# Kernel optimization log

Hardware: AMD Instinct MI355X
Metric: run time of the kernel (lower is better)

## Reference

```python
import jax, jax.numpy as jnp
import numpy as np

EPS = 1e-5  # torch BatchNorm2d default eps (eval mode with running stats)


def bn(x, g, b, m, v):
    # x: [B,C,H,W]; per-channel affine batchnorm in inference form
    return (x - m[:, None, None]) * (g[:, None, None] / jnp.sqrt(v[:, None, None] + EPS)) + b[:, None, None]


def self_attn(x, Wq, bq, Wk, bk, Wv, bv, rel_h, rel_w):
    # x: [B,C,H,W]; Wq/Wk/Wv: [C,C] (1x1 convs); rel_h: [C,H]; rel_w: [C,W]
    B, C, H, W = x.shape
    N = H * W
    q = jnp.einsum('oc,bchw->bohw', Wq, x).reshape(B, C, N) + bq[None, :, None]
    k = jnp.einsum('oc,bchw->bohw', Wk, x).reshape(B, C, N) + bk[None, :, None]
    v = jnp.einsum('oc,bchw->bohw', Wv, x).reshape(B, C, N) + bv[None, :, None]
    energy = jnp.einsum('bcn,bcm->bnm', q, k)                      # content: Q^T K
    pos = (rel_h[:, :, None] + rel_w[:, None, :]).reshape(C, N)    # [C, H*W]
    energy = energy + jnp.einsum('bcn,cm->bnm', q, pos)            # rel-pos bias term
    attn = jax.nn.softmax(energy, axis=-1)                         # [B,N,N]
    out = jnp.einsum('bcm,bnm->bcn', v, attn)                      # V @ attn^T
    return out.reshape(B, C, H, W)


def conv3x3(x, w):
    return jax.lax.conv_general_dilated(x, w, (1, 1), 'SAME',
                                        dimension_numbers=('NCHW', 'OIHW', 'NCHW'))


def setup_inputs() -> dict:
    key = jax.random.key(0)
    B, C, H, W, NH = 32, 512, 16, 16, 5
    ks = jax.random.split(key, 32)
    f = lambda i, shape, s=1.0: jax.random.normal(ks[i], shape, jnp.float32) * s
    inp = {
        'x0': f(0, (B, C, H, W)), 'x1': f(1, (B, C, H, W)), 'x2': f(2, (B, C, H, W)),
        'x3': f(3, (B, C, H, W)), 'x': f(4, (B, C, H, W)),
        'qW': f(5, (NH, C, C), 0.02), 'qB': f(6, (NH, C), 0.02),
        'kW': f(7, (NH, C, C), 0.02), 'kB': f(8, (NH, C), 0.02),
        'vW': f(9, (NH, C, C), 0.02), 'vB': f(10, (NH, C), 0.02),
        'relH': f(11, (NH, C, H)), 'relW': f(12, (NH, C, W)),
        'msw_W': f(13, (NH - 1, NH * C), 0.02),
        'msw_g': jnp.ones((NH - 1,)), 'msw_b': jnp.zeros((NH - 1,)),
        'msw_m': jnp.zeros((NH - 1,)), 'msw_v': jnp.ones((NH - 1,)),
        'fus_W': f(14, (C, C, 3, 3), 0.02),
        'fus_g': jnp.ones((C,)), 'fus_b': jnp.zeros((C,)),
        'fus_m': jnp.zeros((C,)), 'fus_v': jnp.ones((C,)),
        'top_g': jnp.ones((C,)), 'top_b': jnp.zeros((C,)),
        'top_m': jnp.zeros((C,)), 'top_v': jnp.ones((C,)),
        'h': 16, 'w': 16,
    }
    return inp


def reference(x0, x1, x2, x3, x, qW, qB, kW, kB, vW, vB, relH, relW,
              msw_W, msw_g, msw_b, msw_m, msw_v,
              fus_W, fus_g, fus_b, fus_m, fus_v,
              top_g, top_b, top_m, top_v, h, w):
    B, C, H, W = x.shape
    xs = jnp.stack([x0, x1, x2, x3, x])                            # [5,B,C,H,W]
    outs = jax.vmap(self_attn)(xs, qW, qB, kW, kB, vW, vB, relH, relW)  # [5,B,C,H,W]
    cat = outs.transpose(1, 0, 2, 3, 4).reshape(B, 5 * C, H, W)
    weights = jax.nn.sigmoid(bn(jnp.einsum('oc,bchw->bohw', msw_W, cat),
                                msw_g, msw_b, msw_m, msw_v))        # [B,4,H,W]
    x_ms = (weights[:, 0:1] * outs[0] + weights[:, 1:2] * outs[1]
            + weights[:, 2:3] * outs[2] + weights[:, 3:4] * outs[3] + outs[4])
    x_ms = jax.nn.relu(bn(conv3x3(x_ms, fus_W), fus_g, fus_b, fus_m, fus_v))
    out = jax.nn.relu(bn(x_ms + x, top_g, top_b, top_m, top_v))
    return out
```

## Files before the change

### kernel.cpp

```cpp
#include <hip/hip_runtime.h>
#include <cstdint>

using bf16x8  = __attribute__((ext_vector_type(8))) __bf16;
using f32x4   = __attribute__((ext_vector_type(4))) float;
using ushort8 = __attribute__((ext_vector_type(8))) unsigned short;

#define EPSN 1e-5f

__device__ __forceinline__ void gld16(const void* g, void* l) {
  __builtin_amdgcn_global_load_lds((const __attribute__((address_space(1))) void*)g,
                                   (__attribute__((address_space(3))) void*)l, 16, 0, 0);
}

__device__ __forceinline__ ushort f2bf(float f) {
  __bf16 h = (__bf16)f;
  return __builtin_bit_cast(unsigned short, h);
}
__device__ __forceinline__ float bf2f(ushort u) {
  union { uint32_t u; float f; } v; v.u = ((uint32_t)u) << 16; return v.f;
}

__device__ __forceinline__ void gemm_core(const ushort* __restrict__ Ag,
                                          const ushort* __restrict__ Bg,
                                          int ldk, int ksteps,
                                          ushort* As, ushort* Bs,
                                          f32x4 (&acc)[4][4]) {
  const int t = threadIdx.x, lane = t & 63, w = t >> 6;
  const int wr = w >> 1, wc = w & 1;
  for (int kt = 0; kt < ksteps; ++kt) {
    const int kbase = kt * 64;
#pragma unroll
    for (int p = 0; p < 4; ++p) {
      int q = p * 256 + t;
      int row = q >> 3, slot = q & 7;
      int srcs = slot ^ (row & 7);
      gld16(Ag + (size_t)row * ldk + kbase + srcs * 8, As + (p * 256 + w * 64) * 8);
      gld16(Bg + (size_t)row * ldk + kbase + srcs * 8, Bs + (p * 256 + w * 64) * 8);
    }
    __syncthreads();
#pragma unroll
    for (int kk = 0; kk < 2; ++kk) {
      bf16x8 af[4], bfv[4];
#pragma unroll
      for (int i = 0; i < 4; ++i) {
        int ra = wr * 64 + i * 16 + (lane & 15);
        int sa = (kk * 4 + (lane >> 4)) ^ (ra & 7);
        af[i] = *(const bf16x8*)(As + ra * 64 + sa * 8);
        int rb = wc * 64 + i * 16 + (lane & 15);
        int sb = (kk * 4 + (lane >> 4)) ^ (rb & 7);
        bfv[i] = *(const bf16x8*)(Bs + rb * 64 + sb * 8);
      }
#pragma unroll
      for (int i = 0; i < 4; ++i)
#pragma unroll
        for (int j = 0; j < 4; ++j)
          acc[i][j] = __builtin_amdgcn_mfma_f32_16x16x32_bf16(af[i], bfv[j], acc[i][j], 0, 0, 0);
    }
    __syncthreads();
  }
}

__global__ __launch_bounds__(256) void k_pre(const float* __restrict__ x0,
                                             const float* __restrict__ x1,
                                             const float* __restrict__ x2,
                                             const float* __restrict__ x3,
                                             const float* __restrict__ x4,
                                             const float* __restrict__ qW,
                                             const float* __restrict__ kW,
                                             const float* __restrict__ vW,
                                             const float* __restrict__ relH,
                                             const float* __restrict__ relW,
                                             ushort* __restrict__ xT,
                                             ushort* __restrict__ Wb,
                                             ushort* __restrict__ posb) {
  __shared__ float tile[64][65];
  int bid = blockIdx.x;
  const int t = threadIdx.x;
  if (bid < 5120) {
    const int nt4 = bid & 3;  bid >>= 2;
    const int ct  = bid & 7;  bid >>= 3;
    const int b   = bid & 31; bid >>= 5;
    const int ix  = bid;
    const float* xs = ix == 0 ? x0 : ix == 1 ? x1 : ix == 2 ? x2 : ix == 3 ? x3 : x4;
    const float* src = xs + ((size_t)b * 512 + ct * 64) * 256 + nt4 * 64;
    const int col = t & 63, rq = t >> 6;
#pragma unroll
    for (int rr = 0; rr < 16; ++rr) {
      int row = rr * 4 + rq;
      tile[row][col] = src[(size_t)row * 256 + col];
    }
    __syncthreads();
    ushort* dst = xT + ((size_t)(ix * 32 + b) * 256 + nt4 * 64) * 512 + ct * 64;
#pragma unroll
    for (int rr = 0; rr < 16; ++rr) {
      int nrow = rr * 4 + rq;
      dst[(size_t)nrow * 512 + col] = f2bf(tile[col][nrow]);
    }
  } else if (bid < 8960) {
    int idx = (bid - 5120) * 256 + t;
    int gi = idx * 4;
    int sel = gi / 1310720;
    int off = gi - sel * 1310720;
    const float* src = sel == 0 ? qW : (sel == 1 ? kW : vW);
    float4 vv = *(const float4*)(src + off);
    int h = off / 262144, rest = off - h * 262144;
    ushort4 o;
    o.x = f2bf(vv.x); o.y = f2bf(vv.y); o.z = f2bf(vv.z); o.w = f2bf(vv.w);
    *(ushort4*)(Wb + (size_t)(h * 3 + sel) * 262144 + rest) = o;
  } else {
    int idx8 = (bid - 8960) * 256 + t;
    int e0 = idx8 * 8;
    int c0 = e0 & 511, m = (e0 >> 9) & 255, h = e0 >> 17;
    ushort8 o;
#pragma unroll
    for (int e = 0; e < 8; ++e) {
      int c = c0 + e;
      o[e] = f2bf(relH[((size_t)h * 512 + c) * 16 + (m >> 4)] +
                  relW[((size_t)h * 512 + c) * 16 + (m & 15)]);
    }
    *(ushort8*)(posb + e0) = o;
  }
}

__global__ __launch_bounds__(512, 2) void k_qkv2(const ushort* __restrict__ Wb,
                                                 const ushort* __restrict__ xT,
                                                 const ushort* __restrict__ posb,
                                                 const float* __restrict__ qB,
                                                 const float* __restrict__ kB,
                                                 const float* __restrict__ vB,
                                                 ushort* __restrict__ qT,
                                                 ushort* __restrict__ kpT,
                                                 ushort* __restrict__ vv) {
  extern __shared__ ushort ls[];
  const int t = threadIdx.x, lane = t & 63;
  const int w = t >> 6, wm = w >> 2, wn = w & 3, g = lane >> 4, l = lane & 15;
  int bid = blockIdx.x;
  bid = (bid & 7) * 120 + (bid >> 3);
  const int h = bid / 192;
  const int r = bid % 192;

  const ushort* Ag;
  const ushort* Bg;
  const bool partA = r < 128;
  int pt = 0, nt = 0, mt = 0, ntv = 0;
  if (partA) {
    pt = r >> 2; nt = r & 3;
    Ag = xT + ((size_t)h * 8192 + pt * 256) * 512;
    const int sel = nt < 2 ? 0 : 1;
    Bg = Wb + ((size_t)(h * 3 + sel) * 512 + (nt & 1) * 256) * 512;
  } else {
    const int r2 = r - 128;
    mt = r2 >> 5; ntv = r2 & 31;
    Ag = Wb + ((size_t)(h * 3 + 2) * 512 + mt * 256) * 512;
    Bg = xT + ((size_t)h * 8192 + ntv * 256) * 512;
  }

  f32x4 acc[8][4];
#pragma unroll
  for (int i = 0; i < 8; ++i)
#pragma unroll
    for (int j = 0; j < 4; ++j) acc[i][j] = f32x4{0.f, 0.f, 0.f, 0.f};

#define QKV_STAGE(tt, slot)                                                    \
  {                                                                            \
    const int kb_ = (tt) * 32;                                                 \
    ushort* sa_ = ls + (slot) * 8192;                                          \
    ushort* sb_ = ls + 32768 + (slot) * 8192;                                  \
    _Pragma("unroll")                                                          \
    for (int p_ = 0; p_ < 2; ++p_) {                                           \
      int q_ = p_ * 512 + t;                                                   \
      int row_ = q_ >> 2, s4_ = q_ & 3;                                        \
      int src_ = s4_ ^ ((row_ ^ (row_ >> 2)) & 3);                             \
      gld16(Ag + (size_t)row_ * 512 + kb_ + src_ * 8, sa_ + q_ * 8);           \
      gld16(Bg + (size_t)row_ * 512 + kb_ + src_ * 8, sb_ + q_ * 8);           \
    }                                                                          \
  }

#define QKV_COMPUTE(slot)                                                      \
  {                                                                            \
    ushort* sa_ = ls + (slot) * 8192;                                          \
    ushort* sb_ = ls + 32768 + (slot) * 8192;                                  \
    bf16x8 bfv[4], af[8];                                                      \
    _Pragma("unroll")                                                          \
    for (int j_ = 0; j_ < 4; ++j_) {                                           \
      int rb_ = wn * 64 + j_ * 16 + l;                                         \
      int sb2_ = g ^ ((rb_ ^ (rb_ >> 2)) & 3);                                 \
      bfv[j_] = *(const bf16x8*)(sb_ + rb_ * 32 + sb2_ * 8);                   \
    }                                                                          \
    _Pragma("unroll")                                                          \
    for (int i_ = 0; i_ < 8; ++i_) {                                           \
      int ra_ = wm * 128 + i_ * 16 + l;                                        \
      int sa2_ = g ^ ((ra_ ^ (ra_ >> 2)) & 3);                                 \
      af[i_] = *(const bf16x8*)(sa_ + ra_ * 32 + sa2_ * 8);                    \
    }                                                                          \
    asm volatile("s_waitcnt lgkmcnt(0)" ::: "memory");                         \
    __builtin_amdgcn_sched_barrier(0);                                         \
    __builtin_amdgcn_s_setprio(1);                                             \
    _Pragma("unroll")                                                          \
    for (int i_ = 0; i_ < 8; ++i_)                                             \
      _Pragma("unroll")                                                        \
      for (int j_ = 0; j_ < 4; ++j_)                                           \
        acc[i_][j_] = __builtin_amdgcn_mfma_f32_16x16x32_bf16(af[i_], bfv[j_], \
                                                              acc[i_][j_], 0, 0, 0); \
    __builtin_amdgcn_s_setprio(0);                                             \
  }

  QKV_STAGE(0, 0);
  QKV_STAGE(1, 1);
  for (int tt = 0; tt < 14; ++tt) {
    QKV_STAGE(tt + 2, (tt + 2) & 3);
    __builtin_amdgcn_sched_barrier(0);
    asm volatile("s_waitcnt vmcnt(8)" ::: "memory");
    __builtin_amdgcn_s_barrier();
    __builtin_amdgcn_sched_barrier(0);
    QKV_COMPUTE(tt & 3);
  }
  __builtin_amdgcn_sched_barrier(0);
  asm volatile("s_waitcnt vmcnt(4)" ::: "memory");
  __builtin_amdgcn_s_barrier();
  __builtin_amdgcn_sched_barrier(0);
  QKV_COMPUTE(2);
  __builtin_amdgcn_sched_barrier(0);
  asm volatile("s_waitcnt vmcnt(0)" ::: "memory");
  __builtin_amdgcn_s_barrier();
  __builtin_amdgcn_sched_barrier(0);
  QKV_COMPUTE(3);
  __builtin_amdgcn_sched_barrier(0);
  __syncthreads();

  ushort(*Cs)[272] = (ushort(*)[272])ls;
  if (partA) {
    const bool isq = nt < 2;
    const float* bias = (isq ? qB : kB) + (size_t)h * 512 + (nt & 1) * 256;
    ushort* dst = isq ? qT : kpT;
    float bj[4];
#pragma unroll
    for (int j = 0; j < 4; ++j) bj[j] = bias[wn * 64 + j * 16 + l];
#pragma unroll
    for (int R = 0; R < 2; ++R) {
      if (wm == R) {
#pragma unroll
        for (int i = 0; i < 8; ++i)
#pragma unroll
          for (int j = 0; j < 4; ++j)
#pragma unroll
            for (int rr = 0; rr < 4; ++rr)
              Cs[i * 16 + g * 4 + rr][wn * 64 + j * 16 + l] = f2bf(acc[i][j][rr] + bj[j]);
      }
      __syncthreads();
#pragma unroll
      for (int it = 0; it < 8; ++it) {
        int lin = it * 512 + t;
        int row = lin >> 5, cc8 = (lin & 31) * 8;
        ushort8 cv = *(const ushort8*)&Cs[row][cc8];
        if (!isq) {
          ushort8 pv = *(const ushort8*)(posb + ((size_t)h * 256 + R * 128 + row) * 512 +
                                         (nt & 1) * 256 + cc8);
#pragma unroll
          for (int e = 0; e < 8; ++e) cv[e] = f2bf(bf2f(cv[e]) + bf2f(pv[e]));
        }
        *(ushort8*)(dst + ((size_t)h * 8192 + pt * 256 + R * 128 + row) * 512 +
                    (nt & 1) * 256 + cc8) = cv;
      }
      if (R == 0) __syncthreads();
    }
  } else {
    const float* bias = vB + (size_t)h * 512 + mt * 256;
#pragma unroll
    for (int R = 0; R < 2; ++R) {
      if (wm == R) {
#pragma unroll
        for (int i = 0; i < 8; ++i) {
          float4 b4 = *(const float4*)(bias + R * 128 + i * 16 + g * 4);
#pragma unroll
          for (int j = 0; j < 4; ++j)
#pragma unroll
            for (int rr = 0; rr < 4; ++rr)
              Cs[i * 16 + g * 4 + rr][wn * 64 + j * 16 + l] =
                  f2bf(acc[i][j][rr] + ((const float*)&b4)[rr]);
        }
      }
      __syncthreads();
#pragma unroll
      for (int it = 0; it < 8; ++it) {
        int lin = it * 512 + t;
        int row = lin >> 5, cc8 = (lin & 31) * 8;
        ushort8 cv = *(const ushort8*)&Cs[row][cc8];
        *(ushort8*)(vv + (((size_t)(h * 32 + ntv)) * 512 + mt * 256 + R * 128 + row) * 256 +
                    cc8) = cv;
      }
      if (R == 0) __syncthreads();
    }
  }
#undef QKV_STAGE
#undef QKV_COMPUTE
}

__global__ __launch_bounds__(256) void k_attn(const ushort* __restrict__ qT,
                                              const ushort* __restrict__ kpT,
                                              const float* __restrict__ fusW,
                                              ushort* __restrict__ attn,
                                              ushort* __restrict__ Wconv) {
  __shared__ ushort sm[20480];
  __shared__ float red[4][64];
  __shared__ float comb[64];
  int bid = blockIdx.x;
  const int t = threadIdx.x;
  if (bid >= 640) {
    int p = (bid - 640) * 256 + t;
    const float* src = fusW + (size_t)p * 9;
    float vv[9];
#pragma unroll
    for (int s = 0; s < 9; ++s) vv[s] = src[s];
#pragma unroll
    for (int s = 0; s < 9; ++s) Wconv[(size_t)s * 262144 + p] = f2bf(vv[s]);
    return;
  }
  bid = (bid & 7) * 80 + (bid >> 3);
  const int rt = bid & 3;
  const int hb = bid >> 2;
  ushort* As = sm;
  ushort* Bs = sm + 4096;
  const ushort* Ag = qT + ((size_t)hb * 256 + rt * 64) * 512;
  const ushort* Bg = kpT + (size_t)hb * 256 * 512;
  const int lane = t & 63, w = t >> 6, g = lane >> 4, l = lane & 15;

  f32x4 acc[4][4];
#pragma unroll
  for (int i = 0; i < 4; ++i)
#pragma unroll
    for (int j = 0; j < 4; ++j) acc[i][j] = f32x4{0.f, 0.f, 0.f, 0.f};

  for (int kt = 0; kt < 8; ++kt) {
    const int kbase = kt * 64;
#pragma unroll
    for (int p = 0; p < 2; ++p) {
      int q = p * 256 + t;
      int row = q >> 3, slot = q & 7, srcs = slot ^ (row & 7);
      gld16(Ag + (size_t)row * 512 + kbase + srcs * 8, As + (p * 256 + w * 64) * 8);
    }
#pragma unroll
    for (int p = 0; p < 8; ++p) {
      int q = p * 256 + t;
      int row = q >> 3, slot = q & 7, srcs = slot ^ (row & 7);
      gld16(Bg + (size_t)row * 512 + kbase + srcs * 8, Bs + (p * 256 + w * 64) * 8);
    }
    __syncthreads();
#pragma unroll
    for (int kk = 0; kk < 2; ++kk) {
      bf16x8 af[4], bfv[4];
#pragma unroll
      for (int i = 0; i < 4; ++i) {
        int ra = i * 16 + l;
        int sa = (kk * 4 + g) ^ (ra & 7);
        af[i] = *(const bf16x8*)(As + ra * 64 + sa * 8);
        int rb = w * 64 + i * 16 + l;
        int sb = (kk * 4 + g) ^ (rb & 7);
        bfv[i] = *(const bf16x8*)(Bs + rb * 64 + sb * 8);
      }
#pragma unroll
      for (int i = 0; i < 4; ++i)
#pragma unroll
        for (int j = 0; j < 4; ++j)
          acc[i][j] = __builtin_amdgcn_mfma_f32_16x16x32_bf16(af[i], bfv[j], acc[i][j], 0, 0, 0);
    }
    __syncthreads();
  }

#pragma unroll
  for (int i = 0; i < 4; ++i)
#pragma unroll
    for (int rr = 0; rr < 4; ++rr) {
      float v = fmaxf(fmaxf(acc[i][0][rr], acc[i][1][rr]), fmaxf(acc[i][2][rr], acc[i][3][rr]));
#pragma unroll
      for (int m = 1; m < 16; m <<= 1) v = fmaxf(v, __shfl_xor(v, m));
      if (l == 0) red[w][i * 16 + g * 4 + rr] = v;
    }
  __syncthreads();
  if (t < 64) comb[t] = fmaxf(fmaxf(red[0][t], red[1][t]), fmaxf(red[2][t], red[3][t]));
  __syncthreads();
#pragma unroll
  for (int i = 0; i < 4; ++i)
#pragma unroll
    for (int rr = 0; rr < 4; ++rr) {
      float mx = comb[i * 16 + g * 4 + rr];
      float s = 0.f;
#pragma unroll
      for (int j = 0; j < 4; ++j) {
        float e = expf(acc[i][j][rr] - mx);
        acc[i][j][rr] = e;
        s += e;
      }
#pragma unroll
      for (int m = 1; m < 16; m <<= 1) s += __shfl_xor(s, m);
      if (l == 0) red[w][i * 16 + g * 4 + rr] = s;
    }
  __syncthreads();
  if (t < 64) comb[t] = red[0][t] + red[1][t] + red[2][t] + red[3][t];
  __syncthreads();
  ushort(*P)[260] = (ushort(*)[260])sm;
#pragma unroll
  for (int i = 0; i < 4; ++i)
#pragma unroll
    for (int rr = 0; rr < 4; ++rr) {
      int row = i * 16 + g * 4 + rr;
      float inv = 1.f / comb[row];
#pragma unroll
      for (int j = 0; j < 4; ++j)
        P[row][w * 64 + j * 16 + l] = f2bf(acc[i][j][rr] * inv);
    }
  __syncthreads();
  ushort* Arow = attn + (size_t)hb * 65536 + (size_t)rt * 16384;
#pragma unroll
  for (int it = 0; it < 8; ++it) {
    int lin = it * 256 + t;
    int row = lin >> 5, c8 = (lin & 31) * 8;
    ushort8 cv = *(const ushort8*)&P[row][c8];
    *(ushort8*)(Arow + (size_t)row * 256 + c8) = cv;
  }
}

__global__ __launch_bounds__(256) void k_pv(const ushort* __restrict__ attn,
                                            const ushort* __restrict__ vv,
                                            ushort* __restrict__ OT) {
  __shared__ ushort lds[128 * 148];
  ushort* As = lds;
  ushort* Bs = lds + 8192;
  int bid = blockIdx.x;
  bid = (bid & 7) * 160 + (bid >> 3);
  const int nt = bid & 3; bid >>= 2;
  const int mt = bid & 1; bid >>= 1;
  const size_t hb = (size_t)bid;
  const ushort* Ag = attn + (hb * 256 + mt * 128) * 256;
  const ushort* Bg = vv + (hb * 512 + nt * 128) * 256;
  f32x4 acc[4][4];
#pragma unroll
  for (int i = 0; i < 4; ++i)
#pragma unroll
    for (int j = 0; j < 4; ++j) acc[i][j] = f32x4{0.f, 0.f, 0.f, 0.f};
  gemm_core(Ag, Bg, 256, 4, As, Bs, acc);
  const int t = threadIdx.x, lane = t & 63, w = t >> 6;
  const int wr = w >> 1, wc = w & 1, g = lane >> 4, l = lane & 15;
  ushort(*Cs)[148] = (ushort(*)[148])lds;
#pragma unroll
  for (int i = 0; i < 4; ++i)
#pragma unroll
    for (int j = 0; j < 4; ++j)
#pragma unroll
      for (int rr = 0; rr < 4; ++rr)
        Cs[wr * 64 + i * 16 + g * 4 + rr][wc * 64 + j * 16 + l] = f2bf(acc[i][j][rr]);
  __syncthreads();
#pragma unroll
  for (int it = 0; it < 8; ++it) {
    int lin = it * 256 + t;
    int row = lin >> 4, cc = (lin & 15) * 8;
    ushort8 cv = *(const ushort8*)&Cs[row][cc];
    *(ushort8*)(OT + (hb * 256 + mt * 128 + row) * 512 + nt * 128 + cc) = cv;
  }
}

__global__ __launch_bounds__(256) void k_weights(const ushort* __restrict__ OT,
                                                 const float* __restrict__ mswW,
                                                 const float* __restrict__ mg,
                                                 const float* __restrict__ mb,
                                                 const float* __restrict__ mm,
                                                 const float* __restrict__ mv,
                                                 ushort* __restrict__ xmsT) {
  __shared__ float msw[10240];
  const int t = threadIdx.x, lane = t & 63, w = t >> 6;
#pragma unroll
  for (int it = 0; it < 10; ++it) {
    int idx = it * 1024 + t * 4;
    *(float4*)(msw + idx) = *(const float4*)(mswW + idx);
  }
  __syncthreads();
  const size_t pix = (size_t)blockIdx.x * 4 + w;
  float o[5][2][4];
#pragma unroll
  for (int h = 0; h < 5; ++h)
#pragma unroll
    for (int hf = 0; hf < 2; ++hf) {
      ushort4 v = *(const ushort4*)(OT + ((size_t)h * 8192 + pix) * 512 + hf * 256 + lane * 4);
      o[h][hf][0] = bf2f(v.x); o[h][hf][1] = bf2f(v.y);
      o[h][hf][2] = bf2f(v.z); o[h][hf][3] = bf2f(v.w);
    }
  float a[4] = {0.f, 0.f, 0.f, 0.f};
#pragma unroll
  for (int j = 0; j < 4; ++j)
#pragma unroll
    for (int h = 0; h < 5; ++h)
#pragma unroll
      for (int hf = 0; hf < 2; ++hf) {
        float4 m4 = *(const float4*)(msw + j * 2560 + h * 512 + hf * 256 + lane * 4);
        a[j] += m4.x * o[h][hf][0] + m4.y * o[h][hf][1] +
                m4.z * o[h][hf][2] + m4.w * o[h][hf][3];
      }
#pragma unroll
  for (int m = 1; m < 64; m <<= 1) {
    a[0] += __shfl_xor(a[0], m); a[1] += __shfl_xor(a[1], m);
    a[2] += __shfl_xor(a[2], m); a[3] += __shfl_xor(a[3], m);
  }
  float wj[4];
#pragma unroll
  for (int j = 0; j < 4; ++j) {
    float val = (a[j] - mm[j]) * (mg[j] * rsqrtf(mv[j] + EPSN)) + mb[j];
    wj[j] = 1.f / (1.f + expf(-val));
  }
#pragma unroll
  for (int hf = 0; hf < 2; ++hf) {
    float r0 = wj[0] * o[0][hf][0] + wj[1] * o[1][hf][0] + wj[2] * o[2][hf][0] + wj[3] * o[3][hf][0] + o[4][hf][0];
    float r1 = wj[0] * o[0][hf][1] + wj[1] * o[1][hf][1] + wj[2] * o[2][hf][1] + wj[3] * o[3][hf][1] + o[4][hf][1];
    float r2 = wj[0] * o[0][hf][2] + wj[1] * o[1][hf][2] + wj[2] * o[2][hf][2] + wj[3] * o[3][hf][2] + o[4][hf][2];
    float r3 = wj[0] * o[0][hf][3] + wj[1] * o[1][hf][3] + wj[2] * o[2][hf][3] + wj[3] * o[3][hf][3] + o[4][hf][3];
    ushort4 pk; pk.x = f2bf(r0); pk.y = f2bf(r1); pk.z = f2bf(r2); pk.w = f2bf(r3);
    *(ushort4*)(xmsT + pix * 512 + hf * 256 + lane * 4) = pk;
  }
}

__global__ __launch_bounds__(256) void k_conv(const ushort* __restrict__ Wconv,
                                              const ushort* __restrict__ xmsT,
                                              float* __restrict__ y1a,
                                              float* __restrict__ y1b) {
  __shared__ ushort As3[3 * 128 * 64];
  __shared__ ushort xp[180 * 76];
  int bid = blockIdx.x;
  bid = (bid & 7) * 64 + (bid >> 3);
  const int ntl = bid & 1; bid >>= 1;
  const int mt = bid & 3;  bid >>= 2;
  const int halfk = bid & 1; bid >>= 1;
  const int bb = bid;
  const int y0 = ntl * 8;
  const int t = threadIdx.x, lane = t & 63, w = t >> 6, wr = w >> 1, wc = w & 1;
  f32x4 acc[4][4];
#pragma unroll
  for (int i = 0; i < 4; ++i)
#pragma unroll
    for (int j = 0; j < 4; ++j) acc[i][j] = f32x4{0.f, 0.f, 0.f, 0.f};

  for (int cb = halfk * 4; cb < halfk * 4 + 4; ++cb) {
    __syncthreads();
    for (int u = t; u < 1440; u += 256) {
      int slot = u & 7;
      int xpi = (u >> 3) % 18;
      int rl = u / 144;
      int yg = y0 - 1 + rl, xg = xpi - 1;
      uint4 val = make_uint4(0, 0, 0, 0);
      if (yg >= 0 && yg < 16 && (unsigned)xg < 16u)
        val = *(const uint4*)(xmsT + ((size_t)bb * 256 + yg * 16 + xg) * 512 + cb * 64 + slot * 8);
      *(uint4*)(xp + (rl * 18 + xpi) * 76 + slot * 8) = val;
    }
    for (int dy = 0; dy < 3; ++dy) {
#pragma unroll
      for (int dx = 0; dx < 3; ++dx)
#pragma unroll
        for (int p = 0; p < 4; ++p) {
          int q = p * 256 + t;
          int row = q >> 3, slot = q & 7, srcs = slot ^ (row & 7);
          gld16(Wconv + ((size_t)(dy * 3 + dx) * 512 + mt * 128 + row) * 512 + cb * 64 + srcs * 8,
                As3 + dx * 8192 + (p * 256 + w * 64) * 8);
        }
      __syncthreads();
#pragma unroll
      for (int dx = 0; dx < 3; ++dx)
#pragma unroll
        for (int kk = 0; kk < 2; ++kk) {
          bf16x8 af[4], bfv[4];
#pragma unroll
          for (int i = 0; i < 4; ++i) {
            int ra = wr * 64 + i * 16 + (lane & 15);
            int sa = (kk * 4 + (lane >> 4)) ^ (ra & 7);
            af[i] = *(const bf16x8*)(As3 + dx * 8192 + ra * 64 + sa * 8);
            int nl = wc * 64 + i * 16 + (lane & 15);
            int pp = ((nl >> 4) + dy) * 18 + (nl & 15) + dx;
            bfv[i] = *(const bf16x8*)(xp + pp * 76 + (kk * 4 + (lane >> 4)) * 8);
          }
#pragma unroll
          for (int i = 0; i < 4; ++i)
#pragma unroll
            for (int j = 0; j < 4; ++j)
              acc[i][j] = __builtin_amdgcn_mfma_f32_16x16x32_bf16(af[i], bfv[j], acc[i][j], 0, 0, 0);
        }
      __syncthreads();
    }
  }
  float* yp = halfk ? y1b : y1a;
  const int o0 = mt * 128 + wr * 64 + ((lane >> 4) << 2);
  const int n0 = ntl * 128 + wc * 64 + (lane & 15);
#pragma unroll
  for (int i = 0; i < 4; ++i)
#pragma unroll
    for (int j = 0; j < 4; ++j)
#pragma unroll
      for (int rr = 0; rr < 4; ++rr) {
        int o = o0 + i * 16 + rr, n = n0 + j * 16;
        yp[((size_t)bb * 512 + o) * 256 + n] = acc[i][j][rr];
      }
}

__global__ __launch_bounds__(256) void k_top(const float* __restrict__ y1a,
                                             const float* __restrict__ y1b,
                                             const float* __restrict__ x,
                                             const float* __restrict__ fg,
                                             const float* __restrict__ fb,
                                             const float* __restrict__ fm,
                                             const float* __restrict__ fv,
                                             const float* __restrict__ tg,
                                             const float* __restrict__ tb,
                                             const float* __restrict__ tm,
                                             const float* __restrict__ tv,
                                             float* __restrict__ out) {
  size_t i4 = ((size_t)blockIdx.x * 256 + threadIdx.x) * 4;
  int c = (int)((i4 >> 8) & 511);
  float4 a = *(const float4*)(y1a + i4);
  float4 bq = *(const float4*)(y1b + i4);
  float4 xx = *(const float4*)(x + i4);
  float sf = fg[c] * rsqrtf(fv[c] + EPSN), mf = fm[c], bf_ = fb[c];
  float st = tg[c] * rsqrtf(tv[c] + EPSN), mt_ = tm[c], bt_ = tb[c];
  float4 o;
  float v;
  v = fmaxf((a.x + bq.x - mf) * sf + bf_, 0.f); o.x = fmaxf((v + xx.x - mt_) * st + bt_, 0.f);
  v = fmaxf((a.y + bq.y - mf) * sf + bf_, 0.f); o.y = fmaxf((v + xx.y - mt_) * st + bt_, 0.f);
  v = fmaxf((a.z + bq.z - mf) * sf + bf_, 0.f); o.z = fmaxf((v + xx.z - mt_) * st + bt_, 0.f);
  v = fmaxf((a.w + bq.w - mf) * sf + bf_, 0.f); o.w = fmaxf((v + xx.w - mt_) * st + bt_, 0.f);
  *(float4*)(out + i4) = o;
}

extern "C" void kernel_launch(void* const* d_in, const int* in_sizes, int n_in,
                              void* d_out, int out_size, void* d_ws, size_t ws_size,
                              hipStream_t stream) {
  const float* x0   = (const float*)d_in[0];
  const float* x1   = (const float*)d_in[1];
  const float* x2   = (const float*)d_in[2];
  const float* x3   = (const float*)d_in[3];
  const float* x4   = (const float*)d_in[4];
  const float* qW   = (const float*)d_in[5];
  const float* qB   = (const float*)d_in[6];
  const float* kW   = (const float*)d_in[7];
  const float* kB   = (const float*)d_in[8];
  const float* vW   = (const float*)d_in[9];
  const float* vB   = (const float*)d_in[10];
  const float* relH = (const float*)d_in[11];
  const float* relW = (const float*)d_in[12];
  const float* mswW = (const float*)d_in[13];
  const float* msg  = (const float*)d_in[14];
  const float* msb  = (const float*)d_in[15];
  const float* msm  = (const float*)d_in[16];
  const float* msv  = (const float*)d_in[17];
  const float* fusW = (const float*)d_in[18];
  const float* fg   = (const float*)d_in[19];
  const float* fb   = (const float*)d_in[20];
  const float* fm   = (const float*)d_in[21];
  const float* fv   = (const float*)d_in[22];
  const float* tg   = (const float*)d_in[23];
  const float* tb   = (const float*)d_in[24];
  const float* tm   = (const float*)d_in[25];
  const float* tv   = (const float*)d_in[26];

  if (ws_size < 180355072ull) return;
  char* ws = (char*)d_ws;
  ushort* xT    = (ushort*)(ws + 0);
  ushort* attn  = (ushort*)(ws + 0);
  ushort* Wconv = (ushort*)(ws + 20971520);
  ushort* qT    = (ushort*)(ws + 41943040);
  ushort* xmsT  = (ushort*)(ws + 41943040);
  float*  y1a   = (float*)(ws + 50331648);
  float*  y1b   = (float*)(ws + 67108864);
  ushort* kpT   = (ushort*)(ws + 83886080);
  ushort* OT    = (ushort*)(ws + 83886080);
  ushort* vv    = (ushort*)(ws + 125829120);
  ushort* Wb    = (ushort*)(ws + 167772160);
  ushort* posb  = (ushort*)(ws + 175636480);

  hipFuncSetAttribute((const void*)k_qkv2,
                      hipFuncAttributeMaxDynamicSharedMemorySize, 131072);

  k_pre    <<<9280, 256, 0, stream>>>(x0, x1, x2, x3, x4, qW, kW, vW, relH, relW,
                                      xT, Wb, posb);
  k_qkv2   <<<960, 512, 131072, stream>>>(Wb, xT, posb, qB, kB, vB, qT, kpT, vv);
  k_attn   <<<1664, 256, 0, stream>>>(qT, kpT, fusW, attn, Wconv);
  k_pv     <<<1280, 256, 0, stream>>>(attn, vv, OT);
  k_weights<<<2048, 256, 0, stream>>>(OT, mswW, msg, msb, msm, msv, xmsT);
  k_conv   <<<512,  256, 0, stream>>>(Wconv, xmsT, y1a, y1b);
  k_top    <<<4096, 256, 0, stream>>>(y1a, y1b, x4, fg, fb, fm, fv, tg, tb, tm, tv, (float*)d_out);
}
```

Baseline: 267.6 us.

## Shrink QKV GEMM tiles to 128x256 with double buffering for higher occupancy

The QKV projection kernel moves from 256x256 output tiles with a 4-stage LDS pipeline and 128KB dynamic shared memory to 128x256 tiles with a 2-stage pipeline using 48KB, doubling the grid to 1920 blocks. Launch bounds now allow 4 blocks per CU, which is meant to raise occupancy and hide latency through more resident waves rather than deeper prefetch. The cost is lower arithmetic intensity per tile, more redundant loads of the B operand, and a shallower prefetch with an extra barrier per k-step.

Result: faster. 256.1 us (-4.3%).

```diff
diff --git a/kernel.cpp b/kernel.cpp
--- a/kernel.cpp
+++ b/kernel.cpp
@@ -122,7 +122,7 @@
   }
 }
 
-__global__ __launch_bounds__(512, 2) void k_qkv2(const ushort* __restrict__ Wb,
+__global__ __launch_bounds__(512, 4) void k_qkv3(const ushort* __restrict__ Wb,
                                                  const ushort* __restrict__ xT,
                                                  const ushort* __restrict__ posb,
                                                  const float* __restrict__ qB,
@@ -135,52 +135,56 @@
   const int t = threadIdx.x, lane = t & 63;
   const int w = t >> 6, wm = w >> 2, wn = w & 3, g = lane >> 4, l = lane & 15;
   int bid = blockIdx.x;
-  bid = (bid & 7) * 120 + (bid >> 3);
-  const int h = bid / 192;
-  const int r = bid % 192;
+  bid = (bid & 7) * 240 + (bid >> 3);
+  const int h = bid / 384;
+  const int r = bid % 384;
 
   const ushort* Ag;
   const ushort* Bg;
-  const bool partA = r < 128;
+  const bool partA = r < 256;
   int pt = 0, nt = 0, mt = 0, ntv = 0;
   if (partA) {
     pt = r >> 2; nt = r & 3;
-    Ag = xT + ((size_t)h * 8192 + pt * 256) * 512;
-    const int sel = nt < 2 ? 0 : 1;
-    Bg = Wb + ((size_t)(h * 3 + sel) * 512 + (nt & 1) * 256) * 512;
+    Ag = xT + ((size_t)h * 8192 + pt * 128) * 512;
+    Bg = Wb + ((size_t)(h * 3 + (nt >> 1)) * 512 + (nt & 1) * 256) * 512;
   } else {
-    const int r2 = r - 128;
+    const int r2 = r - 256;
     mt = r2 >> 5; ntv = r2 & 31;
-    Ag = Wb + ((size_t)(h * 3 + 2) * 512 + mt * 256) * 512;
+    Ag = Wb + ((size_t)(h * 3 + 2) * 512 + mt * 128) * 512;
     Bg = xT + ((size_t)h * 8192 + ntv * 256) * 512;
   }
 
-  f32x4 acc[8][4];
-#pragma unroll
-  for (int i = 0; i < 8; ++i)
+  f32x4 acc[4][4];
+#pragma unroll
+  for (int i = 0; i < 4; ++i)
 #pragma unroll
     for (int j = 0; j < 4; ++j) acc[i][j] = f32x4{0.f, 0.f, 0.f, 0.f};
 
 #define QKV_STAGE(tt, slot)                                                    \
   {                                                                            \
     const int kb_ = (tt) * 32;                                                 \
-    ushort* sa_ = ls + (slot) * 8192;                                          \
-    ushort* sb_ = ls + 32768 + (slot) * 8192;                                  \
+    ushort* sa_ = ls + (slot) * 4096;                                          \
+    ushort* sb_ = ls + 8192 + (slot) * 8192;                                   \
+    {                                                                          \
+      int q_ = t;                                                              \
+      int row_ = q_ >> 2, s4_ = q_ & 3;                                        \
+      int src_ = s4_ ^ ((row_ ^ (row_ >> 2)) & 3);                             \
+      gld16(Ag + (size_t)row_ * 512 + kb_ + src_ * 8, sa_ + q_ * 8);           \
+    }                                                                          \
     _Pragma("unroll")                                                          \
     for (int p_ = 0; p_ < 2; ++p_) {                                           \
       int q_ = p_ * 512 + t;                                                   \
       int row_ = q_ >> 2, s4_ = q_ & 3;                                        \
       int src_ = s4_ ^ ((row_ ^ (row_ >> 2)) & 3);                             \
-      gld16(Ag + (size_t)row_ * 512 + kb_ + src_ * 8, sa_ + q_ * 8);           \
       gld16(Bg + (size_t)row_ * 512 + kb_ + src_ * 8, sb_ + q_ * 8);           \
     }                                                                          \
   }
 
 #define QKV_COMPUTE(slot)                                                      \
   {                                                                            \
-    ushort* sa_ = ls + (slot) * 8192;                                          \
-    ushort* sb_ = ls + 32768 + (slot) * 8192;                                  \
-    bf16x8 bfv[4], af[8];                                                      \
+    ushort* sa_ = ls + (slot) * 4096;                                          \
+    ushort* sb_ = ls + 8192 + (slot) * 8192;                                   \
+    bf16x8 af[4], bfv[4];                                                      \
     _Pragma("unroll")                                                          \
     for (int j_ = 0; j_ < 4; ++j_) {                                           \
       int rb_ = wn * 64 + j_ * 16 + l;                                         \
@@ -188,8 +192,8 @@
       bfv[j_] = *(const bf16x8*)(sb_ + rb_ * 32 + sb2_ * 8);                   \
     }                                                                          \
     _Pragma("unroll")                                                          \
-    for (int i_ = 0; i_ < 8; ++i_) {                                           \
-      int ra_ = wm * 128 + i_ * 16 + l;                                        \
+    for (int i_ = 0; i_ < 4; ++i_) {                                           \
+      int ra_ = wm * 64 + i_ * 16 + l;                                         \
       int sa2_ = g ^ ((ra_ ^ (ra_ >> 2)) & 3);                                 \
       af[i_] = *(const bf16x8*)(sa_ + ra_ * 32 + sa2_ * 8);                    \
     }                                                                          \
@@ -197,7 +201,7 @@
     __builtin_amdgcn_sched_barrier(0);                                         \
     __builtin_amdgcn_s_setprio(1);                                             \
     _Pragma("unroll")                                                          \
-    for (int i_ = 0; i_ < 8; ++i_)                                             \
+    for (int i_ = 0; i_ < 4; ++i_)                                             \
       _Pragma("unroll")                                                        \
       for (int j_ = 0; j_ < 4; ++j_)                                           \
         acc[i_][j_] = __builtin_amdgcn_mfma_f32_16x16x32_bf16(af[i_], bfv[j_], \
@@ -206,29 +210,23 @@
   }
 
   QKV_STAGE(0, 0);
-  QKV_STAGE(1, 1);
-  for (int tt = 0; tt < 14; ++tt) {
-    QKV_STAGE(tt + 2, (tt + 2) & 3);
+  for (int tt = 0; tt < 15; ++tt) {
+    __builtin_amdgcn_s_barrier();
+    QKV_STAGE(tt + 1, (tt + 1) & 1);
     __builtin_amdgcn_sched_barrier(0);
-    asm volatile("s_waitcnt vmcnt(8)" ::: "memory");
+    asm volatile("s_waitcnt vmcnt(3)" ::: "memory");
     __builtin_amdgcn_s_barrier();
     __builtin_amdgcn_sched_barrier(0);
-    QKV_COMPUTE(tt & 3);
-  }
-  __builtin_amdgcn_sched_barrier(0);
-  asm volatile("s_waitcnt vmcnt(4)" ::: "memory");
-  __builtin_amdgcn_s_barrier();
-  __builtin_amdgcn_sched_barrier(0);
-  QKV_COMPUTE(2);
+    QKV_COMPUTE(tt & 1);
+  }
   __builtin_amdgcn_sched_barrier(0);
   asm volatile("s_waitcnt vmcnt(0)" ::: "memory");
   __builtin_amdgcn_s_barrier();
   __builtin_amdgcn_sched_barrier(0);
-  QKV_COMPUTE(3);
-  __builtin_amdgcn_sched_barrier(0);
-  __syncthreads();
-
-  ushort(*Cs)[272] = (ushort(*)[272])ls;
+  QKV_COMPUTE(1);
+  __syncthreads();
+
+  ushort(*Cs)[260] = (ushort(*)[260])ls;
   if (partA) {
     const bool isq = nt < 2;
     const float* bias = (isq ? qB : kB) + (size_t)h * 512 + (nt & 1) * 256;
@@ -240,7 +238,7 @@
     for (int R = 0; R < 2; ++R) {
       if (wm == R) {
 #pragma unroll
-        for (int i = 0; i < 8; ++i)
+        for (int i = 0; i < 4; ++i)
 #pragma unroll
           for (int j = 0; j < 4; ++j)
 #pragma unroll
@@ -249,29 +247,29 @@
       }
       __syncthreads();
 #pragma unroll
-      for (int it = 0; it < 8; ++it) {
+      for (int it = 0; it < 4; ++it) {
         int lin = it * 512 + t;
         int row = lin >> 5, cc8 = (lin & 31) * 8;
+        int pglob = pt * 128 + R * 64 + row;
         ushort8 cv = *(const ushort8*)&Cs[row][cc8];
         if (!isq) {
-          ushort8 pv = *(const ushort8*)(posb + ((size_t)h * 256 + R * 128 + row) * 512 +
+          ushort8 pv = *(const ushort8*)(posb + ((size_t)h * 256 + (pglob & 255)) * 512 +
                                          (nt & 1) * 256 + cc8);
 #pragma unroll
           for (int e = 0; e < 8; ++e) cv[e] = f2bf(bf2f(cv[e]) + bf2f(pv[e]));
         }
-        *(ushort8*)(dst + ((size_t)h * 8192 + pt * 256 + R * 128 + row) * 512 +
-                    (nt & 1) * 256 + cc8) = cv;
+        *(ushort8*)(dst + ((size_t)h * 8192 + pglob) * 512 + (nt & 1) * 256 + cc8) = cv;
       }
       if (R == 0) __syncthreads();
     }
   } else {
-    const float* bias = vB + (size_t)h * 512 + mt * 256;
+    const float* bias = vB + (size_t)h * 512 + mt * 128;
 #pragma unroll
     for (int R = 0; R < 2; ++R) {
       if (wm == R) {
 #pragma unroll
-        for (int i = 0; i < 8; ++i) {
-          float4 b4 = *(const float4*)(bias + R * 128 + i * 16 + g * 4);
+        for (int i = 0; i < 4; ++i) {
+          float4 b4 = *(const float4*)(bias + R * 64 + i * 16 + g * 4);
 #pragma unroll
           for (int j = 0; j < 4; ++j)
 #pragma unroll
@@ -282,12 +280,12 @@
       }
       __syncthreads();
 #pragma unroll
-      for (int it = 0; it < 8; ++it) {
+      for (int it = 0; it < 4; ++it) {
         int lin = it * 512 + t;
         int row = lin >> 5, cc8 = (lin & 31) * 8;
+        int og = mt * 128 + R * 64 + row;
         ushort8 cv = *(const ushort8*)&Cs[row][cc8];
-        *(ushort8*)(vv + (((size_t)(h * 32 + ntv)) * 512 + mt * 256 + R * 128 + row) * 256 +
-                    cc8) = cv;
+        *(ushort8*)(vv + (((size_t)(h * 32 + ntv)) * 512 + og) * 256 + cc8) = cv;
       }
       if (R == 0) __syncthreads();
     }
@@ -671,12 +669,9 @@
   ushort* Wb    = (ushort*)(ws + 167772160);
   ushort* posb  = (ushort*)(ws + 175636480);
 
-  hipFuncSetAttribute((const void*)k_qkv2,
-                      hipFuncAttributeMaxDynamicSharedMemorySize, 131072);
-
   k_pre    <<<9280, 256, 0, stream>>>(x0, x1, x2, x3, x4, qW, kW, vW, relH, relW,
                                       xT, Wb, posb);
-  k_qkv2   <<<960, 512, 131072, stream>>>(Wb, xT, posb, qB, kB, vB, qT, kpT, vv);
+  k_qkv3   <<<1920, 512, 49152, stream>>>(Wb, xT, posb, qB, kB, vB, qT, kpT, vv);
   k_attn   <<<1664, 256, 0, stream>>>(qT, kpT, fusW, attn, Wconv);
   k_pv     <<<1280, 256, 0, stream>>>(attn, vv, OT);
   k_weights<<<2048, 256, 0, stream>>>(OT, mswW, msg, msb, msm, msv, xmsT);
```
